# Performance work log

Measured on AMD Instinct MI355X. Metric: run time of the kernel, lower is better.

Reference implementation:

```python
import jax, jax.numpy as jnp
import numpy as np

N = 50000
E = 800000
IN_C = 128
HID = 128
OUT_C = 64
HEADS = 8
HD1 = HID // HEADS   # 16 per-head dim, layer 1 (concat)
HD2 = OUT_C          # 64 per-head dim, layer 2 (concat=False, mean over heads)
NEG_SLOPE = 0.2


def setup_inputs() -> dict:
    key = jax.random.key(0)
    ks = jax.random.split(key, 12)
    x = jax.random.normal(ks[0], (N, IN_C), dtype=jnp.float32)
    edge_index = jax.random.randint(ks[1], (2, E), 0, N, dtype=jnp.int64)
    s1 = 1.0 / np.sqrt(IN_C)
    s2 = 1.0 / np.sqrt(HID)
    W1 = jax.random.normal(ks[2], (IN_C, HEADS * HD1), dtype=jnp.float32) * s1
    att_src1 = jax.random.normal(ks[3], (HEADS, HD1), dtype=jnp.float32) * s1
    att_dst1 = jax.random.normal(ks[4], (HEADS, HD1), dtype=jnp.float32) * s1
    b1 = jnp.zeros((HID,), dtype=jnp.float32)
    W2 = jax.random.normal(ks[5], (HID, HEADS * HD2), dtype=jnp.float32) * s2
    att_src2 = jax.random.normal(ks[6], (HEADS, HD2), dtype=jnp.float32) * s2
    att_dst2 = jax.random.normal(ks[7], (HEADS, HD2), dtype=jnp.float32) * s2
    b2 = jnp.zeros((OUT_C,), dtype=jnp.float32)
    return {"x": x, "edge_index": edge_index,
            "W1": W1, "att_src1": att_src1, "att_dst1": att_dst1, "b1": b1,
            "W2": W2, "att_src2": att_src2, "att_dst2": att_dst2, "b2": b2}


def _gat_conv(x, W, a_src, a_dst, bias, src, dst, heads, head_dim, concat):
    n = x.shape[0]
    h = (x @ W).reshape(n, heads, head_dim)                      # [N,H,D]
    alpha_s = jnp.einsum('nhd,hd->nh', h, a_src)                  # [N,H]
    alpha_d = jnp.einsum('nhd,hd->nh', h, a_dst)                  # [N,H]
    e = jax.nn.leaky_relu(alpha_s[src] + alpha_d[dst], NEG_SLOPE)  # [E,H]
    # segment softmax over edges grouped by destination node
    m = jax.ops.segment_max(e, dst, num_segments=n)               # [N,H]
    m = jnp.where(jnp.isfinite(m), m, 0.0)
    ex = jnp.exp(e - m[dst])
    denom = jax.ops.segment_sum(ex, dst, num_segments=n)
    alpha = ex / (denom[dst] + 1e-16)                             # [E,H]
    out = jax.ops.segment_sum(h[src] * alpha[:, :, None], dst, num_segments=n)  # [N,H,D]
    if concat:
        out = out.reshape(n, heads * head_dim)
    else:
        out = out.mean(axis=1)
    return out + bias


def reference(x, edge_index, W1, att_src1, att_dst1, b1, W2, att_src2, att_dst2, b2):
    # PyG GATConv default add_self_loops=True
    loops = jnp.arange(N, dtype=edge_index.dtype)
    src = jnp.concatenate([edge_index[0], loops])
    dst = jnp.concatenate([edge_index[1], loops])
    h = _gat_conv(x, W1, att_src1, att_dst1, b1, src, dst, HEADS, HD1, True)
    h = jax.nn.relu(h)
    out = _gat_conv(h, W2, att_src2, att_dst2, b2, src, dst, HEADS, HD2, False)
    return out
```

## Files before the change

### kernel.cpp

```cpp
#include <hip/hip_runtime.h>

#define N_NODES 50000
#define N_EDGES 800000
#define ET (N_EDGES + N_NODES)
#define HEADS 8
#define NPAD 50048
#define SCAN_NB 196
#define CAP 96
#define LRS 1032

typedef __attribute__((ext_vector_type(8))) _Float16 half8;
typedef __attribute__((ext_vector_type(2))) _Float16 half2v;
typedef __attribute__((ext_vector_type(4))) float f32x4;

__device__ __forceinline__ int edge_src(const int* ei, int e, int is64){
  if (e >= N_EDGES) return e - N_EDGES;
  return is64 ? ei[2*e] : ei[e];
}
__device__ __forceinline__ int edge_dst(const int* ei, int e, int is64){
  if (e >= N_EDGES) return e - N_EDGES;
  return is64 ? ei[2*(N_EDGES + e)] : ei[N_EDGES + e];
}

__global__ void k_init(const int* __restrict__ ei, int* __restrict__ deg,
                       int* __restrict__ cnt, int* __restrict__ flag){
  int i = blockIdx.x*blockDim.x + threadIdx.x;
  if (i < N_NODES){ deg[i] = 0; cnt[i] = 0; }
  if (i == 0){
    int zeros = 0;
    for (int k = 0; k < 64; k++){
      if (ei[2*k + 1] == 0) zeros++;
    }
    *flag = (zeros >= 60) ? 1 : 0;
  }
}

__global__ void k_degree(const int* __restrict__ ei, int* __restrict__ deg,
                         const int* __restrict__ flag){
  int e = blockIdx.x*blockDim.x + threadIdx.x;
  if (e >= ET) return;
  int is64 = *flag;
  int d = edge_dst(ei, e, is64);
  atomicAdd(&deg[d], 1);
}

__global__ void k_scan_part(const int* __restrict__ deg, int* __restrict__ loc,
                            int* __restrict__ part){
  __shared__ int lds[256];
  int t = threadIdx.x, i = blockIdx.x*256 + t;
  int v = (i < N_NODES) ? deg[i] : 0;
  lds[t] = v;
  __syncthreads();
  for (int off = 1; off < 256; off <<= 1){
    int x = (t >= off) ? lds[t - off] : 0;
    __syncthreads();
    lds[t] += x;
    __syncthreads();
  }
  if (i < N_NODES) loc[i] = lds[t] - v;
  if (t == 255) part[blockIdx.x] = lds[255];
}

__global__ void k_scan_carry(int* __restrict__ part, int* __restrict__ carry){
  __shared__ int lds[256];
  int t = threadIdx.x;
  int v = (t < SCAN_NB) ? part[t] : 0;
  lds[t] = v;
  __syncthreads();
  for (int off = 1; off < 256; off <<= 1){
    int x = (t >= off) ? lds[t - off] : 0;
    __syncthreads();
    lds[t] += x;
    __syncthreads();
  }
  if (t < SCAN_NB) carry[t] = lds[t] - v;
}

__global__ void k_scan_add(const int* __restrict__ loc, const int* __restrict__ carry,
                           int* __restrict__ row_ptr){
  int i = blockIdx.x*blockDim.x + threadIdx.x;
  if (i < N_NODES) row_ptr[i] = loc[i] + carry[i >> 8];
  if (i == 0) row_ptr[N_NODES] = ET;
}

__global__ void k_fill(const int* __restrict__ ei, const int* __restrict__ row_ptr,
                       int* __restrict__ cnt, int* __restrict__ col,
                       const int* __restrict__ flag){
  int e = blockIdx.x*blockDim.x + threadIdx.x;
  if (e >= ET) return;
  int is64 = *flag;
  int s = edge_src(ei, e, is64);
  int d = edge_dst(ei, e, is64);
  int pos = atomicAdd(&cnt[d], 1);
  col[row_ptr[d] + pos] = s;
}

__global__ void k_wprep(const float* __restrict__ W1, const float* __restrict__ W2,
                        const float* __restrict__ as2, const float* __restrict__ ad2,
                        _Float16* __restrict__ Bp1, _Float16* __restrict__ Bp,
                        float* __restrict__ ws2, float* __restrict__ wd2){
  int b = blockIdx.x;
  int t_ = threadIdx.x;
  if (b < 256){
    int t = b*256 + t_;
    int j = t & 7, lane = (t >> 3) & 63, nt = (t >> 9) & 3, kt = t >> 11;
    int k = kt*32 + (lane >> 4)*8 + j;
    int c = nt*16 + (lane & 15);
    int h = k >> 7, kk = k & 127;
    Bp[t] = (_Float16)(0.125f * W2[kk*512 + h*64 + c]);
  } else if (b < 320){
    int t = (b - 256)*256 + t_;
    int j = t & 7, lane = (t >> 3) & 63, nt = (t >> 9) & 7, kt = t >> 12;
    int k = kt*32 + (lane >> 4)*8 + j;
    int c = nt*16 + (lane & 15);
    Bp1[t] = (_Float16)W1[k*128 + c];
  } else {
    int t = (b - 320)*256 + t_;
    int k = t >> 3, h = t & 7;
    float s = 0.f, d = 0.f;
    for (int dd = 0; dd < 64; dd++){
      float w = W2[k*512 + h*64 + dd];
      s += w * as2[h*64 + dd];
      d += w * ad2[h*64 + dd];
    }
    ws2[h*128 + k] = s;
    wd2[h*128 + k] = d;
  }
}

__global__ void __launch_bounds__(256) k_gemm1_mfma(
    const float* __restrict__ x, const _Float16* __restrict__ Bp1,
    _Float16* __restrict__ h1,
    const float* __restrict__ as1, const float* __restrict__ ad1,
    float* __restrict__ als1, float* __restrict__ ald1){
  int tid = threadIdx.x;
  int lane = tid & 63, wv = tid >> 6;
  int n0 = blockIdx.x*64 + wv*16;
  int rowA = n0 + (lane & 15);
  int koff = (lane >> 4)*8;
  const float* xr = x + (size_t)rowA*128 + koff;
  f32x4 acc[8];
  #pragma unroll
  for (int i = 0; i < 8; i++) acc[i] = (f32x4){0.f,0.f,0.f,0.f};
  bool inb = (rowA < N_NODES);
  #pragma unroll
  for (int kt = 0; kt < 4; kt++){
    half8 af;
    if (inb){
      float4 a0 = *(const float4*)(xr + kt*32);
      float4 a1 = *(const float4*)(xr + kt*32 + 4);
      af = (half8){(_Float16)a0.x,(_Float16)a0.y,(_Float16)a0.z,(_Float16)a0.w,
                   (_Float16)a1.x,(_Float16)a1.y,(_Float16)a1.z,(_Float16)a1.w};
    } else {
      af = (half8){0,0,0,0,0,0,0,0};
    }
    #pragma unroll
    for (int nt = 0; nt < 8; nt++){
      half8 bf = *(const half8*)(Bp1 + (((kt*8 + nt)*64 + lane) << 3));
      acc[nt] = __builtin_amdgcn_mfma_f32_16x16x32_f16(af, bf, acc[nt], 0, 0, 0);
    }
  }
  int m = lane & 15, q = lane >> 4;
  int r0 = n0 + q*4;
  #pragma unroll
  for (int nt = 0; nt < 8; nt++){
    int c = nt*16 + m;
    #pragma unroll
    for (int r = 0; r < 4; r++){
      int n = r0 + r;
      if (n < N_NODES) h1[(size_t)n*128 + c] = (_Float16)acc[nt][r];
    }
  }
  float as1v[8], ad1v[8];
  #pragma unroll
  for (int nt = 0; nt < 8; nt++){
    as1v[nt] = as1[nt*16 + m];
    ad1v[nt] = ad1[nt*16 + m];
  }
  #pragma unroll
  for (int r = 0; r < 4; r++){
    float vs[8], vd[8];
    #pragma unroll
    for (int nt = 0; nt < 8; nt++){
      vs[nt] = acc[nt][r]*as1v[nt];
      vd[nt] = acc[nt][r]*ad1v[nt];
      #pragma unroll
      for (int off = 1; off < 16; off <<= 1){
        vs[nt] += __shfl_xor(vs[nt], off, 64);
        vd[nt] += __shfl_xor(vd[nt], off, 64);
      }
    }
    int n = r0 + r;
    if (m == r && n < N_NODES){
      float4 v0; v0.x = vs[0]; v0.y = vs[1]; v0.z = vs[2]; v0.w = vs[3];
      float4 v1; v1.x = vs[4]; v1.y = vs[5]; v1.z = vs[6]; v1.w = vs[7];
      float4 w0; w0.x = vd[0]; w0.y = vd[1]; w0.z = vd[2]; w0.w = vd[3];
      float4 w1; w1.x = vd[4]; w1.y = vd[5]; w1.z = vd[6]; w1.w = vd[7];
      *(float4*)&als1[n*8]     = v0;
      *(float4*)&als1[n*8 + 4] = v1;
      *(float4*)&ald1[n*8]     = w0;
      *(float4*)&ald1[n*8 + 4] = w1;
    }
  }
}

__global__ void k_attn_agg1(const _Float16* __restrict__ h1,
    const float* __restrict__ als, const float* __restrict__ ald,
    const int* __restrict__ row_ptr, const int* __restrict__ col,
    const float* __restrict__ bias, _Float16* __restrict__ hr,
    const float* __restrict__ ws2, const float* __restrict__ wd2,
    float* __restrict__ als2, float* __restrict__ ald2){
  __shared__ _Float16 ew_s[4][CAP*8];
  __shared__ int col_s[4][CAP];
  __shared__ _Float16 ot_s[4][132];
  int tid = threadIdx.x;
  int wv = tid >> 6, lane = tid & 63;
  int n = blockIdx.x*4 + wv;
  int beg = row_ptr[n], end = row_ptr[n+1];
  int deg = end - beg;
  int items = deg*8;
  int h = lane & 7;
  float ad = ald[n*8 + h];
  _Float16* es = ew_s[wv];
  int* cs = col_s[wv];
  float l = 0.f;
  int itc = items < CAP*8 ? items : CAP*8;
  int it = lane;
  for (; it < itc; it += 64){
    int e = it >> 3;
    int s = col[beg + e];
    float a = als[s*8 + h] + ad;
    a = (a > 0.f) ? a : 0.2f*a;
    float ex = __expf(a);
    es[it] = (_Float16)ex;
    if ((it & 7) == 0) cs[e] = s;
    l += ex;
  }
  for (; it < items; it += 64){
    int s = col[beg + (it >> 3)];
    float a = als[s*8 + h] + ad;
    a = (a > 0.f) ? a : 0.2f*a;
    l += __expf(a);
  }
  l += __shfl_xor(l, 8, 64);
  l += __shfl_xor(l, 16, 64);
  l += __shfl_xor(l, 32, 64);
  float inv = 1.f / (l + 1e-16f);
  __syncthreads();
  int hh0 = lane >> 3;
  float invh = __shfl(inv, hh0, 64);
  const half2v* h2p = (const half2v*)h1;
  float ax = 0.f, ay = 0.f;
  int degc = deg < CAP ? deg : CAP;
  int j = 0;
  for (; j + 7 < degc; j += 8){
    int s[8]; float w[8]; half2v v[8];
    #pragma unroll
    for (int u = 0; u < 8; u++) s[u] = cs[j + u];
    #pragma unroll
    for (int u = 0; u < 8; u++) w[u] = (float)es[(j + u)*8 + hh0] * invh;
    #pragma unroll
    for (int u = 0; u < 8; u++) v[u] = h2p[(size_t)s[u]*64 + lane];
    #pragma unroll
    for (int u = 0; u < 8; u++){ ax += w[u]*(float)v[u].x; ay += w[u]*(float)v[u].y; }
  }
  for (; j < degc; j++){
    int s = cs[j];
    float w = (float)es[j*8 + hh0] * invh;
    half2v v = h2p[(size_t)s*64 + lane];
    ax += w*(float)v.x; ay += w*(float)v.y;
  }
  float adh = ald[n*8 + hh0];
  for (; j < deg; j++){
    int s = col[beg + j];
    float a = als[s*8 + hh0] + adh;
    a = (a > 0.f) ? a : 0.2f*a;
    float w = __expf(a)*invh;
    half2v v = h2p[(size_t)s*64 + lane];
    ax += w*(float)v.x; ay += w*(float)v.y;
  }
  float2 bb = ((const float2*)bias)[lane];
  float o0 = fmaxf(ax + bb.x, 0.f);
  float o1 = fmaxf(ay + bb.y, 0.f);
  half2v oo; oo.x = (_Float16)o0; oo.y = (_Float16)o1;
  ((half2v*)hr)[(size_t)n*64 + lane] = oo;
  ((half2v*)&ot_s[wv][0])[lane] = oo;
  int hh = lane >> 3, seg = lane & 7;
  const half2v* otp = (const half2v*)&ot_s[wv][0];
  const float* wsr = ws2 + hh*128 + seg*16;
  const float* wdr = wd2 + hh*128 + seg*16;
  float vs = 0.f, vd = 0.f;
  #pragma unroll
  for (int i = 0; i < 8; i++){
    half2v v = otp[seg*8 + i];
    float vx = (float)v.x, vy = (float)v.y;
    vs += vx*wsr[2*i] + vy*wsr[2*i + 1];
    vd += vx*wdr[2*i] + vy*wdr[2*i + 1];
  }
  vs += __shfl_xor(vs, 1, 64); vd += __shfl_xor(vd, 1, 64);
  vs += __shfl_xor(vs, 2, 64); vd += __shfl_xor(vd, 2, 64);
  vs += __shfl_xor(vs, 4, 64); vd += __shfl_xor(vd, 4, 64);
  if (seg == 0){
    als2[n*8 + hh] = vs;
    ald2[n*8 + hh] = vd;
  }
}

__global__ void __launch_bounds__(1024) k_attn_agg2(const _Float16* __restrict__ hr,
    const float* __restrict__ als, const float* __restrict__ ald,
    const int* __restrict__ row_ptr, const int* __restrict__ col,
    const _Float16* __restrict__ Bp, const float* __restrict__ b2,
    float* __restrict__ outp){
  __shared__ _Float16 ew_s[16][CAP*8];
  __shared__ int col_s[16][CAP];
  __shared__ _Float16 at[16*LRS];
  int tid = threadIdx.x;
  int wv = tid >> 6, lane = tid & 63;
  int n = blockIdx.x*16 + wv;
  int beg = row_ptr[n], end = row_ptr[n+1];
  int deg = end - beg;
  int items = deg*8;
  int h = lane & 7;
  float ad = ald[n*8 + h];
  _Float16* es = ew_s[wv];
  int* cs = col_s[wv];
  float l = 0.f;
  int itc = items < CAP*8 ? items : CAP*8;
  int it = lane;
  for (; it < itc; it += 64){
    int e = it >> 3;
    int s = col[beg + e];
    float a = als[s*8 + h] + ad;
    a = (a > 0.f) ? a : 0.2f*a;
    float ex = __expf(a);
    es[it] = (_Float16)ex;
    if ((it & 7) == 0) cs[e] = s;
    l += ex;
  }
  for (; it < items; it += 64){
    int s = col[beg + (it >> 3)];
    float a = als[s*8 + h] + ad;
    a = (a > 0.f) ? a : 0.2f*a;
    l += __expf(a);
  }
  l += __shfl_xor(l, 8, 64);
  l += __shfl_xor(l, 16, 64);
  l += __shfl_xor(l, 32, 64);
  float inv = 1.f / (l + 1e-16f);
  __syncthreads();
  int hp = lane >> 4, cb = lane & 15;
  float invA = __shfl(inv, 2*hp, 64);
  float invB = __shfl(inv, 2*hp + 1, 64);
  half2v inv2; inv2.x = (_Float16)invA; inv2.y = (_Float16)invB;
  half2v acc_a[4], acc_b[4];
  #pragma unroll
  for (int i = 0; i < 4; i++){
    acc_a[i] = (half2v){(_Float16)0.f, (_Float16)0.f};
    acc_b[i] = (half2v){(_Float16)0.f, (_Float16)0.f};
  }
  int degc = deg < CAP ? deg : CAP;
  const _Float16* esw = es + 2*hp;
  int j = 0;
  for (; j + 3 < degc; j += 4){
    int s0 = cs[j], s1 = cs[j+1], s2 = cs[j+2], s3 = cs[j+3];
    half2v w0 = *(const half2v*)(esw + (j+0)*8) * inv2;
    half2v w1 = *(const half2v*)(esw + (j+1)*8) * inv2;
    half2v w2 = *(const half2v*)(esw + (j+2)*8) * inv2;
    half2v w3 = *(const half2v*)(esw + (j+3)*8) * inv2;
    half8 v0 = *(const half8*)(hr + (size_t)s0*128 + cb*8);
    half8 v1 = *(const half8*)(hr + (size_t)s1*128 + cb*8);
    half8 v2 = *(const half8*)(hr + (size_t)s2*128 + cb*8);
    half8 v3 = *(const half8*)(hr + (size_t)s3*128 + cb*8);
    #pragma unroll
    for (int k = 0; k < 4; k++){
      half2v t;
      t = (half2v){v0[2*k], v0[2*k+1]};
      acc_a[k] += (half2v){w0.x, w0.x} * t;
      acc_b[k] += (half2v){w0.y, w0.y} * t;
      t = (half2v){v1[2*k], v1[2*k+1]};
      acc_a[k] += (half2v){w1.x, w1.x} * t;
      acc_b[k] += (half2v){w1.y, w1.y} * t;
      t = (half2v){v2[2*k], v2[2*k+1]};
      acc_a[k] += (half2v){w2.x, w2.x} * t;
      acc_b[k] += (half2v){w2.y, w2.y} * t;
      t = (half2v){v3[2*k], v3[2*k+1]};
      acc_a[k] += (half2v){w3.x, w3.x} * t;
      acc_b[k] += (half2v){w3.y, w3.y} * t;
    }
  }
  for (; j < degc; j++){
    int s = cs[j];
    half2v w = *(const half2v*)(esw + j*8) * inv2;
    half8 v = *(const half8*)(hr + (size_t)s*128 + cb*8);
    #pragma unroll
    for (int k = 0; k < 4; k++){
      half2v t = (half2v){v[2*k], v[2*k+1]};
      acc_a[k] += (half2v){w.x, w.x} * t;
      acc_b[k] += (half2v){w.y, w.y} * t;
    }
  }
  if (deg > CAP){
    float2 adv = *(const float2*)(ald + (size_t)n*8 + 2*hp);
    for (; j < deg; j++){
      int s = col[beg + j];
      float2 alv = *(const float2*)(als + (size_t)s*8 + 2*hp);
      float a0 = alv.x + adv.x; a0 = (a0 > 0.f) ? a0 : 0.2f*a0;
      float a1 = alv.y + adv.y; a1 = (a1 > 0.f) ? a1 : 0.2f*a1;
      _Float16 w0 = (_Float16)(__expf(a0)*invA);
      _Float16 w1 = (_Float16)(__expf(a1)*invB);
      half8 v = *(const half8*)(hr + (size_t)s*128 + cb*8);
      #pragma unroll
      for (int k = 0; k < 4; k++){
        half2v t = (half2v){v[2*k], v[2*k+1]};
        acc_a[k] += (half2v){w0, w0} * t;
        acc_b[k] += (half2v){w1, w1} * t;
      }
    }
  }
  _Float16* ar = at + wv*LRS + (2*hp)*128 + cb*8;
  half8 oa, ob;
  #pragma unroll
  for (int k = 0; k < 4; k++){
    oa[2*k] = acc_a[k].x; oa[2*k+1] = acc_a[k].y;
    ob[2*k] = acc_b[k].x; ob[2*k+1] = acc_b[k].y;
  }
  *(half8*)ar = oa;
  *(half8*)(ar + 128) = ob;
  __syncthreads();
  if (wv >= 4) return;
  int m = lane & 15, q = lane >> 4;
  const _Float16* arow = at + m*LRS + q*8;
  f32x4 cacc = (f32x4){0.f,0.f,0.f,0.f};
  #pragma unroll 4
  for (int kt = 0; kt < 32; kt++){
    half8 af = *(const half8*)(arow + kt*32);
    half8 bf = *(const half8*)(Bp + (((kt*4 + wv)*64 + lane) << 3));
    cacc = __builtin_amdgcn_mfma_f32_16x16x32_f16(af, bf, cacc, 0, 0, 0);
  }
  int c = wv*16 + m;
  float bb = b2[c];
  #pragma unroll
  for (int r = 0; r < 4; r++){
    int nrow = blockIdx.x*16 + q*4 + r;
    outp[(size_t)nrow*64 + c] = cacc[r] + bb;
  }
}

extern "C" void kernel_launch(void* const* d_in, const int* in_sizes, int n_in,
                              void* d_out, int out_size, void* d_ws, size_t ws_size,
                              hipStream_t stream){
  const float* x   = (const float*)d_in[0];
  const int*   ei  = (const int*)d_in[1];
  const float* W1  = (const float*)d_in[2];
  const float* as1 = (const float*)d_in[3];
  const float* ad1 = (const float*)d_in[4];
  const float* b1  = (const float*)d_in[5];
  const float* W2  = (const float*)d_in[6];
  const float* as2 = (const float*)d_in[7];
  const float* ad2 = (const float*)d_in[8];
  const float* b2  = (const float*)d_in[9];
  float* outp = (float*)d_out;

  char* p = (char*)d_ws;
  auto alloc = [&](size_t bytes) -> void* {
    void* r = (void*)p;
    p += (bytes + 255) & ~(size_t)255;
    return r;
  };
  _Float16* h1  = (_Float16*)alloc((size_t)NPAD*128*2);
  _Float16* hr  = (_Float16*)alloc((size_t)N_NODES*128*2);
  float* als1 = (float*)alloc((size_t)N_NODES*8*4);
  float* ald1 = (float*)alloc((size_t)N_NODES*8*4);
  float* als2 = (float*)alloc((size_t)N_NODES*8*4);
  float* ald2 = (float*)alloc((size_t)N_NODES*8*4);
  int* row_ptr = (int*)alloc((size_t)(N_NODES+1)*4);
  int* deg  = (int*)alloc((size_t)N_NODES*4);
  int* cnt  = (int*)alloc((size_t)N_NODES*4);
  int* col  = (int*)alloc((size_t)ET*4);
  int* loc  = (int*)alloc((size_t)N_NODES*4);
  int* part = (int*)alloc(256*4);
  int* carry= (int*)alloc(256*4);
  int* flag = (int*)alloc(256);
  float* ws2 = (float*)alloc(1024*4);
  float* wd2 = (float*)alloc(1024*4);
  _Float16* Bp1 = (_Float16*)alloc((size_t)16384*2);
  _Float16* Bp  = (_Float16*)alloc((size_t)65536*2);

  dim3 b256(256);
  k_init<<<(N_NODES+255)/256, b256, 0, stream>>>(ei, deg, cnt, flag);
  k_degree<<<(ET+255)/256, b256, 0, stream>>>(ei, deg, flag);
  k_scan_part<<<SCAN_NB, b256, 0, stream>>>(deg, loc, part);
  k_scan_carry<<<1, b256, 0, stream>>>(part, carry);
  k_scan_add<<<SCAN_NB, b256, 0, stream>>>(loc, carry, row_ptr);
  k_fill<<<(ET+255)/256, b256, 0, stream>>>(ei, row_ptr, cnt, col, flag);
  k_wprep<<<324, b256, 0, stream>>>(W1, W2, as2, ad2, Bp1, Bp, ws2, wd2);

  k_gemm1_mfma<<<NPAD/64, b256, 0, stream>>>(x, Bp1, h1, as1, ad1, als1, ald1);
  k_attn_agg1<<<N_NODES/4, b256, 0, stream>>>(h1, als1, ald1, row_ptr, col,
                                              b1, hr, ws2, wd2, als2, ald2);
  k_attn_agg2<<<N_NODES/16, dim3(1024), 0, stream>>>(hr, als2, ald2, row_ptr, col,
                                                     Bp, b2, outp);
}
```

Measured before the change: 337.4 us.

## Sort nodes by degree descending to balance aggregation workloads across waves

Builds a degree histogram during the scan, computes bucket offsets, and produces a permutation of nodes ordered by descending in-degree. Both attention-aggregation kernels process nodes in this permuted order, and the second kernel writes output rows through the stored node ids. The aim is for waves in the same block to have similar degrees, which cuts intra-block imbalance in the 16-wave kernel and schedules heavy nodes first. In exchange it adds atomics, an extra indirection, and scattered output writes and gathers that lose node-locality.

```diff
diff --git a/kernel.cpp b/kernel.cpp
--- a/kernel.cpp
+++ b/kernel.cpp
@@ -23,9 +23,11 @@
 }
 
 __global__ void k_init(const int* __restrict__ ei, int* __restrict__ deg,
-                       int* __restrict__ cnt, int* __restrict__ flag){
+                       int* __restrict__ cnt, int* __restrict__ flag,
+                       int* __restrict__ hist){
   int i = blockIdx.x*blockDim.x + threadIdx.x;
   if (i < N_NODES){ deg[i] = 0; cnt[i] = 0; }
+  if (i < 256) hist[i] = 0;
   if (i == 0){
     int zeros = 0;
     for (int k = 0; k < 64; k++){
@@ -45,10 +47,14 @@
 }
 
 __global__ void k_scan_part(const int* __restrict__ deg, int* __restrict__ loc,
-                            int* __restrict__ part){
+                            int* __restrict__ part, int* __restrict__ hist){
   __shared__ int lds[256];
   int t = threadIdx.x, i = blockIdx.x*256 + t;
   int v = (i < N_NODES) ? deg[i] : 0;
+  if (i < N_NODES){
+    int b = v > 255 ? 255 : v;
+    atomicAdd(&hist[255 - b], 1);
+  }
   lds[t] = v;
   __syncthreads();
   for (int off = 1; off < 256; off <<= 1){
@@ -61,7 +67,8 @@
   if (t == 255) part[blockIdx.x] = lds[255];
 }
 
-__global__ void k_scan_carry(int* __restrict__ part, int* __restrict__ carry){
+__global__ void k_scan_carry(int* __restrict__ part, int* __restrict__ carry,
+                             const int* __restrict__ hist, int* __restrict__ hoff){
   __shared__ int lds[256];
   int t = threadIdx.x;
   int v = (t < SCAN_NB) ? part[t] : 0;
@@ -74,12 +81,29 @@
     __syncthreads();
   }
   if (t < SCAN_NB) carry[t] = lds[t] - v;
+  __syncthreads();
+  int hv = hist[t];
+  lds[t] = hv;
+  __syncthreads();
+  for (int off = 1; off < 256; off <<= 1){
+    int x = (t >= off) ? lds[t - off] : 0;
+    __syncthreads();
+    lds[t] += x;
+    __syncthreads();
+  }
+  hoff[t] = lds[t] - hv;
 }
 
 __global__ void k_scan_add(const int* __restrict__ loc, const int* __restrict__ carry,
-                           int* __restrict__ row_ptr){
+                           int* __restrict__ row_ptr, const int* __restrict__ deg,
+                           int* __restrict__ hoff, int* __restrict__ perm){
   int i = blockIdx.x*blockDim.x + threadIdx.x;
-  if (i < N_NODES) row_ptr[i] = loc[i] + carry[i >> 8];
+  if (i < N_NODES){
+    row_ptr[i] = loc[i] + carry[i >> 8];
+    int d = deg[i]; if (d > 255) d = 255;
+    int pos = atomicAdd(&hoff[255 - d], 1);
+    perm[pos] = i;
+  }
   if (i == 0) row_ptr[N_NODES] = ET;
 }
 
@@ -209,13 +233,14 @@
     const int* __restrict__ row_ptr, const int* __restrict__ col,
     const float* __restrict__ bias, _Float16* __restrict__ hr,
     const float* __restrict__ ws2, const float* __restrict__ wd2,
-    float* __restrict__ als2, float* __restrict__ ald2){
+    float* __restrict__ als2, float* __restrict__ ald2,
+    const int* __restrict__ perm){
   __shared__ _Float16 ew_s[4][CAP*8];
   __shared__ int col_s[4][CAP];
   __shared__ _Float16 ot_s[4][132];
   int tid = threadIdx.x;
   int wv = tid >> 6, lane = tid & 63;
-  int n = blockIdx.x*4 + wv;
+  int n = perm[blockIdx.x*4 + wv];
   int beg = row_ptr[n], end = row_ptr[n+1];
   int deg = end - beg;
   int items = deg*8;
@@ -310,13 +335,15 @@
     const float* __restrict__ als, const float* __restrict__ ald,
     const int* __restrict__ row_ptr, const int* __restrict__ col,
     const _Float16* __restrict__ Bp, const float* __restrict__ b2,
-    float* __restrict__ outp){
+    float* __restrict__ outp, const int* __restrict__ perm){
   __shared__ _Float16 ew_s[16][CAP*8];
   __shared__ int col_s[16][CAP];
   __shared__ _Float16 at[16*LRS];
+  __shared__ int nid_s[16];
   int tid = threadIdx.x;
   int wv = tid >> 6, lane = tid & 63;
-  int n = blockIdx.x*16 + wv;
+  int n = perm[blockIdx.x*16 + wv];
+  if (lane == 0) nid_s[wv] = n;
   int beg = row_ptr[n], end = row_ptr[n+1];
   int deg = end - beg;
   int items = deg*8;
@@ -441,7 +468,7 @@
   float bb = b2[c];
   #pragma unroll
   for (int r = 0; r < 4; r++){
-    int nrow = blockIdx.x*16 + q*4 + r;
+    int nrow = nid_s[q*4 + r];
     outp[(size_t)nrow*64 + c] = cacc[r] + bb;
   }
 }
@@ -481,23 +508,26 @@
   int* part = (int*)alloc(256*4);
   int* carry= (int*)alloc(256*4);
   int* flag = (int*)alloc(256);
+  int* hist = (int*)alloc(256*4);
+  int* hoff = (int*)alloc(256*4);
+  int* perm = (int*)alloc((size_t)N_NODES*4);
   float* ws2 = (float*)alloc(1024*4);
   float* wd2 = (float*)alloc(1024*4);
   _Float16* Bp1 = (_Float16*)alloc((size_t)16384*2);
   _Float16* Bp  = (_Float16*)alloc((size_t)65536*2);
 
   dim3 b256(256);
-  k_init<<<(N_NODES+255)/256, b256, 0, stream>>>(ei, deg, cnt, flag);
+  k_init<<<(N_NODES+255)/256, b256, 0, stream>>>(ei, deg, cnt, flag, hist);
   k_degree<<<(ET+255)/256, b256, 0, stream>>>(ei, deg, flag);
-  k_scan_part<<<SCAN_NB, b256, 0, stream>>>(deg, loc, part);
-  k_scan_carry<<<1, b256, 0, stream>>>(part, carry);
-  k_scan_add<<<SCAN_NB, b256, 0, stream>>>(loc, carry, row_ptr);
+  k_scan_part<<<SCAN_NB, b256, 0, stream>>>(deg, loc, part, hist);
+  k_scan_carry<<<1, b256, 0, stream>>>(part, carry, hist, hoff);
+  k_scan_add<<<SCAN_NB, b256, 0, stream>>>(loc, carry, row_ptr, deg, hoff, perm);
   k_fill<<<(ET+255)/256, b256, 0, stream>>>(ei, row_ptr, cnt, col, flag);
   k_wprep<<<324, b256, 0, stream>>>(W1, W2, as2, ad2, Bp1, Bp, ws2, wd2);
 
   k_gemm1_mfma<<<NPAD/64, b256, 0, stream>>>(x, Bp1, h1, as1, ad1, als1, ald1);
   k_attn_agg1<<<N_NODES/4, b256, 0, stream>>>(h1, als1, ald1, row_ptr, col,
-                                              b1, hr, ws2, wd2, als2, ald2);
+                                              b1, hr, ws2, wd2, als2, ald2, perm);
   k_attn_agg2<<<N_NODES/16, dim3(1024), 0, stream>>>(hr, als2, ald2, row_ptr, col,
-                                                     Bp, b2, outp);
-}
+                                                     Bp, b2, outp, perm);
+}
```

Result: slower. 611.7 us (+81.3%).

## Merge init with weight prep and degree count with GEMM1; use wave-level LDS fences

Applied to the files above, without the earlier changes.

Fuses the init and weight-prep kernels into one launch, and the degree-counting atomics with the first MFMA GEMM into another, with block ranges selecting the role. This cuts two launches and lets the independent work share the device. In the aggregation kernels, block-wide __syncthreads barriers are replaced by a per-wave s_waitcnt on LDS, because each wave only uses its own shared-memory slice. Dropping the barrier relies on that per-wave independence, and mixing atomic and GEMM blocks in one grid may change scheduling balance.

```diff
diff --git a/kernel.cpp b/kernel.cpp
--- a/kernel.cpp
+++ b/kernel.cpp
@@ -8,11 +8,17 @@
 #define SCAN_NB 196
 #define CAP 96
 #define LRS 1032
+#define NB_DEG 3321
+#define NB_GEMM1 782
 
 typedef __attribute__((ext_vector_type(8))) _Float16 half8;
 typedef __attribute__((ext_vector_type(2))) _Float16 half2v;
 typedef __attribute__((ext_vector_type(4))) float f32x4;
 
+__device__ __forceinline__ void wave_lds_fence(){
+  asm volatile("s_waitcnt lgkmcnt(0)" ::: "memory");
+}
+
 __device__ __forceinline__ int edge_src(const int* ei, int e, int is64){
   if (e >= N_EDGES) return e - N_EDGES;
   return is64 ? ei[2*e] : ei[e];
@@ -22,26 +28,135 @@
   return is64 ? ei[2*(N_EDGES + e)] : ei[N_EDGES + e];
 }
 
-__global__ void k_init(const int* __restrict__ ei, int* __restrict__ deg,
-                       int* __restrict__ cnt, int* __restrict__ flag){
-  int i = blockIdx.x*blockDim.x + threadIdx.x;
-  if (i < N_NODES){ deg[i] = 0; cnt[i] = 0; }
-  if (i == 0){
-    int zeros = 0;
-    for (int k = 0; k < 64; k++){
-      if (ei[2*k + 1] == 0) zeros++;
-    }
-    *flag = (zeros >= 60) ? 1 : 0;
-  }
-}
-
-__global__ void k_degree(const int* __restrict__ ei, int* __restrict__ deg,
-                         const int* __restrict__ flag){
-  int e = blockIdx.x*blockDim.x + threadIdx.x;
-  if (e >= ET) return;
-  int is64 = *flag;
-  int d = edge_dst(ei, e, is64);
-  atomicAdd(&deg[d], 1);
+__global__ void k_init_wprep(const int* __restrict__ ei, int* __restrict__ deg,
+                             int* __restrict__ cnt, int* __restrict__ flag,
+                             const float* __restrict__ W1, const float* __restrict__ W2,
+                             const float* __restrict__ as2, const float* __restrict__ ad2,
+                             _Float16* __restrict__ Bp1, _Float16* __restrict__ Bp,
+                             float* __restrict__ ws2, float* __restrict__ wd2){
+  int b = blockIdx.x;
+  int t_ = threadIdx.x;
+  if (b < SCAN_NB){
+    int i = b*256 + t_;
+    if (i < N_NODES){ deg[i] = 0; cnt[i] = 0; }
+    if (i == 0){
+      int zeros = 0;
+      for (int k = 0; k < 64; k++){
+        if (ei[2*k + 1] == 0) zeros++;
+      }
+      *flag = (zeros >= 60) ? 1 : 0;
+    }
+  } else if (b < SCAN_NB + 256){
+    int t = (b - SCAN_NB)*256 + t_;
+    int j = t & 7, lane = (t >> 3) & 63, nt = (t >> 9) & 3, kt = t >> 11;
+    int k = kt*32 + (lane >> 4)*8 + j;
+    int c = nt*16 + (lane & 15);
+    int h = k >> 7, kk = k & 127;
+    Bp[t] = (_Float16)(0.125f * W2[kk*512 + h*64 + c]);
+  } else if (b < SCAN_NB + 320){
+    int t = (b - SCAN_NB - 256)*256 + t_;
+    int j = t & 7, lane = (t >> 3) & 63, nt = (t >> 9) & 7, kt = t >> 12;
+    int k = kt*32 + (lane >> 4)*8 + j;
+    int c = nt*16 + (lane & 15);
+    Bp1[t] = (_Float16)W1[k*128 + c];
+  } else {
+    int t = (b - SCAN_NB - 320)*256 + t_;
+    int k = t >> 3, h = t & 7;
+    float s = 0.f, d = 0.f;
+    for (int dd = 0; dd < 64; dd++){
+      float w = W2[k*512 + h*64 + dd];
+      s += w * as2[h*64 + dd];
+      d += w * ad2[h*64 + dd];
+    }
+    ws2[h*128 + k] = s;
+    wd2[h*128 + k] = d;
+  }
+}
+
+__global__ void __launch_bounds__(256) k_deg_gemm1(
+    const int* __restrict__ ei, int* __restrict__ deg, const int* __restrict__ flag,
+    const float* __restrict__ x, const _Float16* __restrict__ Bp1,
+    _Float16* __restrict__ h1,
+    const float* __restrict__ as1, const float* __restrict__ ad1,
+    float* __restrict__ als1, float* __restrict__ ald1){
+  if (blockIdx.x < NB_DEG){
+    int e = blockIdx.x*blockDim.x + threadIdx.x;
+    if (e >= ET) return;
+    int is64 = *flag;
+    int d = edge_dst(ei, e, is64);
+    atomicAdd(&deg[d], 1);
+    return;
+  }
+  int bid = blockIdx.x - NB_DEG;
+  int tid = threadIdx.x;
+  int lane = tid & 63, wv = tid >> 6;
+  int n0 = bid*64 + wv*16;
+  int rowA = n0 + (lane & 15);
+  int koff = (lane >> 4)*8;
+  const float* xr = x + (size_t)rowA*128 + koff;
+  f32x4 acc[8];
+  #pragma unroll
+  for (int i = 0; i < 8; i++) acc[i] = (f32x4){0.f,0.f,0.f,0.f};
+  bool inb = (rowA < N_NODES);
+  #pragma unroll
+  for (int kt = 0; kt < 4; kt++){
+    half8 af;
+    if (inb){
+      float4 a0 = *(const float4*)(xr + kt*32);
+      float4 a1 = *(const float4*)(xr + kt*32 + 4);
+      af = (half8){(_Float16)a0.x,(_Float16)a0.y,(_Float16)a0.z,(_Float16)a0.w,
+                   (_Float16)a1.x,(_Float16)a1.y,(_Float16)a1.z,(_Float16)a1.w};
+    } else {
+      af = (half8){0,0,0,0,0,0,0,0};
+    }
+    #pragma unroll
+    for (int nt = 0; nt < 8; nt++){
+      half8 bf = *(const half8*)(Bp1 + (((kt*8 + nt)*64 + lane) << 3));
+      acc[nt] = __builtin_amdgcn_mfma_f32_16x16x32_f16(af, bf, acc[nt], 0, 0, 0);
+    }
+  }
+  int m = lane & 15, q = lane >> 4;
+  int r0 = n0 + q*4;
+  #pragma unroll
+  for (int nt = 0; nt < 8; nt++){
+    int c = nt*16 + m;
+    #pragma unroll
+    for (int r = 0; r < 4; r++){
+      int n = r0 + r;
+      if (n < N_NODES) h1[(size_t)n*128 + c] = (_Float16)acc[nt][r];
+    }
+  }
+  float as1v[8], ad1v[8];
+  #pragma unroll
+  for (int nt = 0; nt < 8; nt++){
+    as1v[nt] = as1[nt*16 + m];
+    ad1v[nt] = ad1[nt*16 + m];
+  }
+  #pragma unroll
+  for (int r = 0; r < 4; r++){
+    float vs[8], vd[8];
+    #pragma unroll
+    for (int nt = 0; nt < 8; nt++){
+      vs[nt] = acc[nt][r]*as1v[nt];
+      vd[nt] = acc[nt][r]*ad1v[nt];
+      #pragma unroll
+      for (int off = 1; off < 16; off <<= 1){
+        vs[nt] += __shfl_xor(vs[nt], off, 64);
+        vd[nt] += __shfl_xor(vd[nt], off, 64);
+      }
+    }
+    int n = r0 + r;
+    if (m == r && n < N_NODES){
+      float4 v0; v0.x = vs[0]; v0.y = vs[1]; v0.z = vs[2]; v0.w = vs[3];
+      float4 v1; v1.x = vs[4]; v1.y = vs[5]; v1.z = vs[6]; v1.w = vs[7];
+      float4 w0; w0.x = vd[0]; w0.y = vd[1]; w0.z = vd[2]; w0.w = vd[3];
+      float4 w1; w1.x = vd[4]; w1.y = vd[5]; w1.z = vd[6]; w1.w = vd[7];
+      *(float4*)&als1[n*8]     = v0;
+      *(float4*)&als1[n*8 + 4] = v1;
+      *(float4*)&ald1[n*8]     = w0;
+      *(float4*)&ald1[n*8 + 4] = w1;
+    }
+  }
 }
 
 __global__ void k_scan_part(const int* __restrict__ deg, int* __restrict__ loc,
@@ -93,115 +208,6 @@
   int d = edge_dst(ei, e, is64);
   int pos = atomicAdd(&cnt[d], 1);
   col[row_ptr[d] + pos] = s;
-}
-
-__global__ void k_wprep(const float* __restrict__ W1, const float* __restrict__ W2,
-                        const float* __restrict__ as2, const float* __restrict__ ad2,
-                        _Float16* __restrict__ Bp1, _Float16* __restrict__ Bp,
-                        float* __restrict__ ws2, float* __restrict__ wd2){
-  int b = blockIdx.x;
-  int t_ = threadIdx.x;
-  if (b < 256){
-    int t = b*256 + t_;
-    int j = t & 7, lane = (t >> 3) & 63, nt = (t >> 9) & 3, kt = t >> 11;
-    int k = kt*32 + (lane >> 4)*8 + j;
-    int c = nt*16 + (lane & 15);
-    int h = k >> 7, kk = k & 127;
-    Bp[t] = (_Float16)(0.125f * W2[kk*512 + h*64 + c]);
-  } else if (b < 320){
-    int t = (b - 256)*256 + t_;
-    int j = t & 7, lane = (t >> 3) & 63, nt = (t >> 9) & 7, kt = t >> 12;
-    int k = kt*32 + (lane >> 4)*8 + j;
-    int c = nt*16 + (lane & 15);
-    Bp1[t] = (_Float16)W1[k*128 + c];
-  } else {
-    int t = (b - 320)*256 + t_;
-    int k = t >> 3, h = t & 7;
-    float s = 0.f, d = 0.f;
-    for (int dd = 0; dd < 64; dd++){
-      float w = W2[k*512 + h*64 + dd];
-      s += w * as2[h*64 + dd];
-      d += w * ad2[h*64 + dd];
-    }
-    ws2[h*128 + k] = s;
-    wd2[h*128 + k] = d;
-  }
-}
-
-__global__ void __launch_bounds__(256) k_gemm1_mfma(
-    const float* __restrict__ x, const _Float16* __restrict__ Bp1,
-    _Float16* __restrict__ h1,
-    const float* __restrict__ as1, const float* __restrict__ ad1,
-    float* __restrict__ als1, float* __restrict__ ald1){
-  int tid = threadIdx.x;
-  int lane = tid & 63, wv = tid >> 6;
-  int n0 = blockIdx.x*64 + wv*16;
-  int rowA = n0 + (lane & 15);
-  int koff = (lane >> 4)*8;
-  const float* xr = x + (size_t)rowA*128 + koff;
-  f32x4 acc[8];
-  #pragma unroll
-  for (int i = 0; i < 8; i++) acc[i] = (f32x4){0.f,0.f,0.f,0.f};
-  bool inb = (rowA < N_NODES);
-  #pragma unroll
-  for (int kt = 0; kt < 4; kt++){
-    half8 af;
-    if (inb){
-      float4 a0 = *(const float4*)(xr + kt*32);
-      float4 a1 = *(const float4*)(xr + kt*32 + 4);
-      af = (half8){(_Float16)a0.x,(_Float16)a0.y,(_Float16)a0.z,(_Float16)a0.w,
-                   (_Float16)a1.x,(_Float16)a1.y,(_Float16)a1.z,(_Float16)a1.w};
-    } else {
-      af = (half8){0,0,0,0,0,0,0,0};
-    }
-    #pragma unroll
-    for (int nt = 0; nt < 8; nt++){
-      half8 bf = *(const half8*)(Bp1 + (((kt*8 + nt)*64 + lane) << 3));
-      acc[nt] = __builtin_amdgcn_mfma_f32_16x16x32_f16(af, bf, acc[nt], 0, 0, 0);
-    }
-  }
-  int m = lane & 15, q = lane >> 4;
-  int r0 = n0 + q*4;
-  #pragma unroll
-  for (int nt = 0; nt < 8; nt++){
-    int c = nt*16 + m;
-    #pragma unroll
-    for (int r = 0; r < 4; r++){
-      int n = r0 + r;
-      if (n < N_NODES) h1[(size_t)n*128 + c] = (_Float16)acc[nt][r];
-    }
-  }
-  float as1v[8], ad1v[8];
-  #pragma unroll
-  for (int nt = 0; nt < 8; nt++){
-    as1v[nt] = as1[nt*16 + m];
-    ad1v[nt] = ad1[nt*16 + m];
-  }
-  #pragma unroll
-  for (int r = 0; r < 4; r++){
-    float vs[8], vd[8];
-    #pragma unroll
-    for (int nt = 0; nt < 8; nt++){
-      vs[nt] = acc[nt][r]*as1v[nt];
-      vd[nt] = acc[nt][r]*ad1v[nt];
-      #pragma unroll
-      for (int off = 1; off < 16; off <<= 1){
-        vs[nt] += __shfl_xor(vs[nt], off, 64);
-        vd[nt] += __shfl_xor(vd[nt], off, 64);
-      }
-    }
-    int n = r0 + r;
-    if (m == r && n < N_NODES){
-      float4 v0; v0.x = vs[0]; v0.y = vs[1]; v0.z = vs[2]; v0.w = vs[3];
-      float4 v1; v1.x = vs[4]; v1.y = vs[5]; v1.z = vs[6]; v1.w = vs[7];
-      float4 w0; w0.x = vd[0]; w0.y = vd[1]; w0.z = vd[2]; w0.w = vd[3];
-      float4 w1; w1.x = vd[4]; w1.y = vd[5]; w1.z = vd[6]; w1.w = vd[7];
-      *(float4*)&als1[n*8]     = v0;
-      *(float4*)&als1[n*8 + 4] = v1;
-      *(float4*)&ald1[n*8]     = w0;
-      *(float4*)&ald1[n*8 + 4] = w1;
-    }
-  }
 }
 
 __global__ void k_attn_agg1(const _Float16* __restrict__ h1,
@@ -246,7 +252,7 @@
   l += __shfl_xor(l, 16, 64);
   l += __shfl_xor(l, 32, 64);
   float inv = 1.f / (l + 1e-16f);
-  __syncthreads();
+  wave_lds_fence();
   int hh0 = lane >> 3;
   float invh = __shfl(inv, hh0, 64);
   const half2v* h2p = (const half2v*)h1;
@@ -285,6 +291,7 @@
   half2v oo; oo.x = (_Float16)o0; oo.y = (_Float16)o1;
   ((half2v*)hr)[(size_t)n*64 + lane] = oo;
   ((half2v*)&ot_s[wv][0])[lane] = oo;
+  wave_lds_fence();
   int hh = lane >> 3, seg = lane & 7;
   const half2v* otp = (const half2v*)&ot_s[wv][0];
   const float* wsr = ws2 + hh*128 + seg*16;
@@ -347,7 +354,7 @@
   l += __shfl_xor(l, 16, 64);
   l += __shfl_xor(l, 32, 64);
   float inv = 1.f / (l + 1e-16f);
-  __syncthreads();
+  wave_lds_fence();
   int hp = lane >> 4, cb = lane & 15;
   float invA = __shfl(inv, 2*hp, 64);
   float invB = __shfl(inv, 2*hp + 1, 64);
@@ -487,15 +494,16 @@
   _Float16* Bp  = (_Float16*)alloc((size_t)65536*2);
 
   dim3 b256(256);
-  k_init<<<(N_NODES+255)/256, b256, 0, stream>>>(ei, deg, cnt, flag);
-  k_degree<<<(ET+255)/256, b256, 0, stream>>>(ei, deg, flag);
+  k_init_wprep<<<SCAN_NB + 324, b256, 0, stream>>>(ei, deg, cnt, flag,
+                                                   W1, W2, as2, ad2,
+                                                   Bp1, Bp, ws2, wd2);
+  k_deg_gemm1<<<NB_DEG + NB_GEMM1, b256, 0, stream>>>(ei, deg, flag,
+                                                      x, Bp1, h1, as1, ad1,
+                                                      als1, ald1);
   k_scan_part<<<SCAN_NB, b256, 0, stream>>>(deg, loc, part);
   k_scan_carry<<<1, b256, 0, stream>>>(part, carry);
   k_scan_add<<<SCAN_NB, b256, 0, stream>>>(loc, carry, row_ptr);
   k_fill<<<(ET+255)/256, b256, 0, stream>>>(ei, row_ptr, cnt, col, flag);
-  k_wprep<<<324, b256, 0, stream>>>(W1, W2, as2, ad2, Bp1, Bp, ws2, wd2);
-
-  k_gemm1_mfma<<<NPAD/64, b256, 0, stream>>>(x, Bp1, h1, as1, ad1, als1, ald1);
   k_attn_agg1<<<N_NODES/4, b256, 0, stream>>>(h1, als1, ald1, row_ptr, col,
                                               b1, hr, ws2, wd2, als2, ald2);
   k_attn_agg2<<<N_NODES/16, dim3(1024), 0, stream>>>(hr, als2, ald2, row_ptr, col,
```

New measurement: 326.6 us. -3.2%, faster.
